# Kernel tuning notes

Measured on AMD Instinct MI355X. Metric: run time of the kernel, lower is better.

The kernel has to match this reference:

```python
import jax, jax.numpy as jnp
import numpy as np

D_MODEL = 1024
NUM_HEADS = 16
HEAD_DIM = D_MODEL // NUM_HEADS
LN_EPS = 1e-5


def setup_inputs() -> dict:
    key = jax.random.key(0)
    ks = jax.random.split(key, 10)
    B, S, D = 4, 2048, D_MODEL
    scale = 1.0 / np.sqrt(D)
    inp = {
        'x': jax.random.normal(ks[0], (B, S, D), dtype=jnp.float32),
        'attention_mask': jnp.ones((B, S), dtype=jnp.float32),
        'Wq': jax.random.normal(ks[1], (D, D), dtype=jnp.float32) * scale,
        'bq': jnp.zeros((D,), dtype=jnp.float32),
        'Wk': jax.random.normal(ks[2], (D, D), dtype=jnp.float32) * scale,
        'bk': jnp.zeros((D,), dtype=jnp.float32),
        'Wv': jax.random.normal(ks[3], (D, D), dtype=jnp.float32) * scale,
        'bv': jnp.zeros((D,), dtype=jnp.float32),
        'Wo': jax.random.normal(ks[4], (D, D), dtype=jnp.float32) * scale,
        'bo': jnp.zeros((D,), dtype=jnp.float32),
        'ln_gamma': jnp.ones((D,), dtype=jnp.float32),
        'ln_beta': jnp.zeros((D,), dtype=jnp.float32),
    }
    return inp


def reference(x, attention_mask, Wq, bq, Wk, bk, Wv, bv, Wo, bo, ln_gamma, ln_beta):
    B, S, D = x.shape
    H, Hd = NUM_HEADS, HEAD_DIM
    identity = x
    # LayerNorm (eps matches torch default 1e-5)
    mu = jnp.mean(x, axis=-1, keepdims=True)
    var = jnp.mean(jnp.square(x - mu), axis=-1, keepdims=True)
    xn = (x - mu) / jnp.sqrt(var + LN_EPS) * ln_gamma + ln_beta
    # projections (torch Linear: x @ W.T + b); weights here stored as [out,in]-compatible square
    q = (xn @ Wq.T + bq).reshape(B, S, H, Hd).transpose(0, 2, 1, 3)  # [B,H,S,Hd]
    k = (xn @ Wk.T + bk).reshape(B, S, H, Hd).transpose(0, 2, 1, 3)
    v = (xn @ Wv.T + bv).reshape(B, S, H, Hd).transpose(0, 2, 1, 3)
    scores = jnp.einsum('bhqd,bhkd->bhqk', q, k) / jnp.sqrt(jnp.float32(Hd))
    # padding mask: [B,S] -> additive [B,1,1,S]
    add_mask = (1.0 - attention_mask)[:, None, None, :] * -10000.0
    scores = scores + add_mask
    # causal mask (strict upper triangle -> -inf)
    causal = jnp.triu(jnp.ones((S, S), dtype=bool), k=1)
    scores = jnp.where(causal[None, None, :, :], -jnp.inf, scores)
    attn = jax.nn.softmax(scores, axis=-1)
    out = jnp.einsum('bhqk,bhkd->bhqd', attn, v)  # [B,H,S,Hd]
    out = out.transpose(0, 2, 1, 3).reshape(B, S, D)
    out = out @ Wo.T + bo
    return identity + out
```

## Files before the change

### kernel.cpp

```cpp
#include <hip/hip_runtime.h>

#define D 1024
#define NH 16
#define HD 64
#define SEQ 2048
#define BATCH 4
#define LN_EPS 1e-5f
#define LOG2E 1.44269504088896f

typedef __attribute__((ext_vector_type(8))) __bf16 bf16x8;
typedef __attribute__((ext_vector_type(4))) float f32x4;

__device__ __forceinline__ ushort f2bf(float f) {
    union { float f; uint u; } c; c.f = f;
    uint u = c.u + 0x7fffu + ((c.u >> 16) & 1u);
    return (ushort)(u >> 16);
}

__device__ __forceinline__ void gl_lds16(const ushort* g, ushort* lds) {
    __builtin_amdgcn_global_load_lds(
        (const __attribute__((address_space(1))) void*)g,
        (__attribute__((address_space(3))) void*)lds, 16, 0, 0);
}

__global__ __launch_bounds__(256) void cvt4(const float* __restrict__ w0,
    const float* __restrict__ w1, const float* __restrict__ w2,
    const float* __restrict__ w3, ushort* __restrict__ out, int n)
{
    int sel = blockIdx.y;
    const float* in = sel == 0 ? w0 : (sel == 1 ? w1 : (sel == 2 ? w2 : w3));
    int i = (blockIdx.x * 256 + threadIdx.x) * 4;
    if (i < n) {
        float4 v = *(const float4*)(in + i);
        ushort4 o;
        o.x = f2bf(v.x); o.y = f2bf(v.y); o.z = f2bf(v.z); o.w = f2bf(v.w);
        *(ushort4*)(out + (size_t)sel * n + i) = o;
    }
}

__global__ __launch_bounds__(256) void ln_kernel(const float* __restrict__ x,
    const float* __restrict__ gamma, const float* __restrict__ beta,
    ushort* __restrict__ xn)
{
    int row = blockIdx.x;
    int tid = threadIdx.x;
    float4 v = ((const float4*)(x + (size_t)row * D))[tid];
    float s = v.x + v.y + v.z + v.w;
#pragma unroll
    for (int off = 32; off > 0; off >>= 1) s += __shfl_down(s, off, 64);
    __shared__ float red1[4], red2[4];
    int wid = tid >> 6, lane = tid & 63;
    if (lane == 0) red1[wid] = s;
    __syncthreads();
    float mean = (red1[0] + red1[1] + red1[2] + red1[3]) * (1.0f / D);
    float dx = v.x - mean, dy = v.y - mean, dz = v.z - mean, dw = v.w - mean;
    float ss = dx * dx + dy * dy + dz * dz + dw * dw;
#pragma unroll
    for (int off = 32; off > 0; off >>= 1) ss += __shfl_down(ss, off, 64);
    if (lane == 0) red2[wid] = ss;
    __syncthreads();
    float var = (red2[0] + red2[1] + red2[2] + red2[3]) * (1.0f / D);
    float rstd = rsqrtf(var + LN_EPS);
    float4 g = ((const float4*)gamma)[tid];
    float4 b = ((const float4*)beta)[tid];
    ushort4 o;
    o.x = f2bf(dx * rstd * g.x + b.x);
    o.y = f2bf(dy * rstd * g.y + b.y);
    o.z = f2bf(dz * rstd * g.z + b.z);
    o.w = f2bf(dw * rstd * g.w + b.w);
    ((ushort4*)(xn + (size_t)row * D))[tid] = o;
}

#define BM 128
#define BKK 64

__global__ __launch_bounds__(256) void gemm_qkv(
    const ushort* __restrict__ A,
    const ushort* __restrict__ W,
    const float* __restrict__ bq, const float* __restrict__ bk,
    const float* __restrict__ bv,
    ushort* __restrict__ Cq, ushort* __restrict__ Ck,
    ushort* __restrict__ CvT,
    int M, int K)
{
    __shared__ ushort As[BM * BKK];
    __shared__ ushort Ws[BM * BKK];
    const int tid = threadIdx.x;
    const int lane = tid & 63;
    const int wave = tid >> 6;
    const int wr = wave >> 1, wc = wave & 1;
    const int m0 = blockIdx.y * BM;
    const int n0g = blockIdx.x * BM;
    const int region = n0g >> 10;
    const int n0l = n0g & 1023;
    const float* bias = region == 0 ? bq : (region == 1 ? bk : bv);
    const int fr = lane & 15, quad = lane >> 4;
    const int r8 = lane >> 3, c8 = lane & 7;
    const int gc8 = c8 ^ r8;
    const int swf = fr & 7;

    const ushort* gA = A + (size_t)(m0 + wave * 32 + r8) * K + gc8 * 8;
    const ushort* gW = W + (size_t)(n0g + wave * 32 + r8) * K + gc8 * 8;
    ushort* ldsA = As + (wave * 32) * BKK;
    ushort* ldsW = Ws + (wave * 32) * BKK;

    f32x4 acc[4][4] = {};

    for (int k0 = 0; k0 < K; k0 += BKK) {
        __syncthreads();
#pragma unroll
        for (int t = 0; t < 4; ++t) {
            gl_lds16(gA + (size_t)t * 8 * K + k0, ldsA + t * 8 * BKK);
            gl_lds16(gW + (size_t)t * 8 * K + k0, ldsW + t * 8 * BKK);
        }
        __syncthreads();
#pragma unroll
        for (int kh = 0; kh < 2; ++kh) {
            bf16x8 af[4], bf[4];
            const int co = ((kh * 4 + quad) ^ swf) * 8;
#pragma unroll
            for (int i = 0; i < 4; ++i) {
                af[i] = *(const bf16x8*)&As[(wr * 64 + i * 16 + fr) * BKK + co];
                bf[i] = *(const bf16x8*)&Ws[(wc * 64 + i * 16 + fr) * BKK + co];
            }
#pragma unroll
            for (int i = 0; i < 4; ++i)
#pragma unroll
                for (int j = 0; j < 4; ++j)
                    acc[i][j] = __builtin_amdgcn_mfma_f32_16x16x32_bf16(af[i], bf[j], acc[i][j], 0, 0, 0);
        }
    }

#pragma unroll
    for (int j = 0; j < 4; ++j) {
        int col = n0l + wc * 64 + j * 16 + fr;
        float bvl = bias[col];
#pragma unroll
        for (int i = 0; i < 4; ++i) {
#pragma unroll
            for (int r = 0; r < 4; ++r) {
                int row = m0 + wr * 64 + i * 16 + quad * 4 + r;
                ushort hv = f2bf(acc[i][j][r] + bvl);
                if (region == 0) {
                    Cq[(size_t)row * 1024 + col] = hv;
                } else if (region == 1) {
                    Ck[(size_t)row * 1024 + col] = hv;
                } else {
                    int bb = row >> 11, s = row & 2047;
                    int hh = col >> 6, d = col & 63;
                    CvT[(((size_t)bb * NH + hh) * HD + d) * SEQ + s] = hv;
                }
            }
        }
    }
}

__global__ __launch_bounds__(256) void gemm_out(
    const ushort* __restrict__ A, const ushort* __restrict__ W,
    const float* __restrict__ bias, const float* __restrict__ resid,
    float* __restrict__ Cf, int M, int N, int K)
{
    __shared__ ushort As[BM * BKK];
    __shared__ ushort Ws[BM * BKK];
    const int tid = threadIdx.x;
    const int lane = tid & 63;
    const int wave = tid >> 6;
    const int wr = wave >> 1, wc = wave & 1;
    const int m0 = blockIdx.y * BM, n0 = blockIdx.x * BM;
    const int fr = lane & 15, quad = lane >> 4;
    const int r8 = lane >> 3, c8 = lane & 7;
    const int gc8 = c8 ^ r8;
    const int swf = fr & 7;

    const ushort* gA = A + (size_t)(m0 + wave * 32 + r8) * K + gc8 * 8;
    const ushort* gW = W + (size_t)(n0 + wave * 32 + r8) * K + gc8 * 8;
    ushort* ldsA = As + (wave * 32) * BKK;
    ushort* ldsW = Ws + (wave * 32) * BKK;

    f32x4 acc[4][4] = {};

    for (int k0 = 0; k0 < K; k0 += BKK) {
        __syncthreads();
#pragma unroll
        for (int t = 0; t < 4; ++t) {
            gl_lds16(gA + (size_t)t * 8 * K + k0, ldsA + t * 8 * BKK);
            gl_lds16(gW + (size_t)t * 8 * K + k0, ldsW + t * 8 * BKK);
        }
        __syncthreads();
#pragma unroll
        for (int kh = 0; kh < 2; ++kh) {
            bf16x8 af[4], bf[4];
            const int co = ((kh * 4 + quad) ^ swf) * 8;
#pragma unroll
            for (int i = 0; i < 4; ++i) {
                af[i] = *(const bf16x8*)&As[(wr * 64 + i * 16 + fr) * BKK + co];
                bf[i] = *(const bf16x8*)&Ws[(wc * 64 + i * 16 + fr) * BKK + co];
            }
#pragma unroll
            for (int i = 0; i < 4; ++i)
#pragma unroll
                for (int j = 0; j < 4; ++j)
                    acc[i][j] = __builtin_amdgcn_mfma_f32_16x16x32_bf16(af[i], bf[j], acc[i][j], 0, 0, 0);
        }
    }

#pragma unroll
    for (int j = 0; j < 4; ++j) {
        int col = n0 + wc * 64 + j * 16 + fr;
        float bvl = bias[col];
#pragma unroll
        for (int i = 0; i < 4; ++i) {
#pragma unroll
            for (int r = 0; r < 4; ++r) {
                int row = m0 + wr * 64 + i * 16 + quad * 4 + r;
                Cf[(size_t)row * N + col] =
                    acc[i][j][r] + bvl + resid[(size_t)row * N + col];
            }
        }
    }
}

#define PSP 72
__global__ __launch_bounds__(256, 3) void flash_mfma(
    const ushort* __restrict__ Q, const ushort* __restrict__ K,
    const ushort* __restrict__ VtG, const float* __restrict__ mask,
    ushort* __restrict__ O)
{
    const int bx = blockIdx.x, h = blockIdx.y, b = blockIdx.z;
    __shared__ ushort Ks[64 * 64];
    __shared__ ushort Vt[64 * 64];
    __shared__ ushort Ps[128 * PSP];
    const int tid = threadIdx.x;
    const int lane = tid & 63, wave = tid >> 6;
    const int fr = lane & 15, quad = lane >> 4;
    const int srow = tid >> 3;
    const int sc8 = tid & 7;
    const int g8 = sc8 ^ (srow & 7);
    const int swf = fr & 7;

    const ushort* gK0 = K + (size_t)(b * SEQ) * D + h * HD + (size_t)srow * D + g8 * 8;
    const ushort* gK1 = gK0 + (size_t)32 * D;
    const ushort* gV0 = VtG + ((size_t)(b * NH + h) * HD + srow) * SEQ + g8 * 8;
    const ushort* gV1 = gV0 + (size_t)32 * SEQ;
    const float* mrow = mask + (size_t)b * SEQ;
    const float SCALE2 = 0.125f * LOG2E;
    const float MASKC = -10000.0f * LOG2E;

    for (int phase = 0; phase < 2; ++phase) {
        const int qt = phase ? (15 - bx) : bx;
        const int q0 = qt * 128;
        bf16x8 qf[2][2];
#pragma unroll
        for (int s = 0; s < 2; ++s) {
            const ushort* qptr = Q + ((size_t)(b * SEQ + q0 + s * 64 + wave * 16 + fr)) * D
                                   + h * HD + quad * 8;
            qf[s][0] = *(const bf16x8*)(qptr);
            qf[s][1] = *(const bf16x8*)(qptr + 32);
        }

        f32x4 oacc[2][4] = {};
        float lsum[2][4] = {};
        const int nkb = 2 * qt + 2;

        for (int kb = 0; kb < nkb; ++kb) {
            __syncthreads();
            gl_lds16(gK0 + (size_t)kb * 64 * D, Ks + wave * 512);
            gl_lds16(gK1 + (size_t)kb * 64 * D, Ks + 2048 + wave * 512);
            gl_lds16(gV0 + kb * 64, Vt + wave * 512);
            gl_lds16(gV1 + kb * 64, Vt + 2048 + wave * 512);
            f32x4 mv[4];
#pragma unroll
            for (int jt = 0; jt < 4; ++jt)
                mv[jt] = ((const f32x4*)(mrow + kb * 64))[jt * 4 + quad];
            __syncthreads();

            const bool s0act = (kb <= 2 * qt);

            f32x4 sacc[2][4] = {};
#pragma unroll
            for (int jt = 0; jt < 4; ++jt) {
                const int rb = (jt * 16 + fr) * 64;
                bf16x8 kf0 = *(const bf16x8*)&Ks[rb + ((quad) ^ swf) * 8];
                bf16x8 kf1 = *(const bf16x8*)&Ks[rb + ((4 + quad) ^ swf) * 8];
                sacc[0][jt] = __builtin_amdgcn_mfma_f32_16x16x32_bf16(kf0, qf[0][0], sacc[0][jt], 0, 0, 0);
                sacc[0][jt] = __builtin_amdgcn_mfma_f32_16x16x32_bf16(kf1, qf[0][1], sacc[0][jt], 0, 0, 0);
                sacc[1][jt] = __builtin_amdgcn_mfma_f32_16x16x32_bf16(kf0, qf[1][0], sacc[1][jt], 0, 0, 0);
                sacc[1][jt] = __builtin_amdgcn_mfma_f32_16x16x32_bf16(kf1, qf[1][1], sacc[1][jt], 0, 0, 0);
            }

            float padd[4][4];
#pragma unroll
            for (int jt = 0; jt < 4; ++jt)
#pragma unroll
                for (int r = 0; r < 4; ++r)
                    padd[jt][r] = fmaf(mv[jt][r], -MASKC, MASKC);
            const int ql = wave * 16 + fr;
#pragma unroll
            for (int s = 0; s < 2; ++s) {
                if (s == 0 && !s0act) continue;
                const bool diag = (kb == 2 * qt + s);
#pragma unroll
                for (int jt = 0; jt < 4; ++jt) {
                    float p[4];
#pragma unroll
                    for (int r = 0; r < 4; ++r) {
                        float v = fmaf(sacc[s][jt][r], SCALE2, padd[jt][r]);
                        if (diag) {
                            int keyl = jt * 16 + quad * 4 + r;
                            v = (keyl > ql) ? -1e30f : v;
                        }
                        float e = exp2f(v);
                        e = __uint_as_float(__float_as_uint(e) & 0xffff0000u);
                        p[r] = e;
                        lsum[s][r] += e;
                    }
                    uint lo = (__float_as_uint(p[0]) >> 16) | (__float_as_uint(p[1]) & 0xffff0000u);
                    uint hi = (__float_as_uint(p[2]) >> 16) | (__float_as_uint(p[3]) & 0xffff0000u);
                    union { uint2 u; ushort4 us; } pu;
                    pu.u.x = lo; pu.u.y = hi;
                    *(ushort4*)&Ps[(s * 64 + wave * 16 + fr) * PSP + jt * 16 + quad * 4] = pu.us;
                }
            }

            bf16x8 pa[2][2];
#pragma unroll
            for (int s = 0; s < 2; ++s) {
                pa[s][0] = *(const bf16x8*)&Ps[(s * 64 + wave * 16 + fr) * PSP + quad * 8];
                pa[s][1] = *(const bf16x8*)&Ps[(s * 64 + wave * 16 + fr) * PSP + 32 + quad * 8];
            }
#pragma unroll
            for (int dt = 0; dt < 4; ++dt) {
                const int rb = (dt * 16 + fr) * 64;
                bf16x8 vf0 = *(const bf16x8*)&Vt[rb + ((quad) ^ swf) * 8];
                bf16x8 vf1 = *(const bf16x8*)&Vt[rb + ((4 + quad) ^ swf) * 8];
                if (s0act) {
                    oacc[0][dt] = __builtin_amdgcn_mfma_f32_16x16x32_bf16(pa[0][0], vf0, oacc[0][dt], 0, 0, 0);
                    oacc[0][dt] = __builtin_amdgcn_mfma_f32_16x16x32_bf16(pa[0][1], vf1, oacc[0][dt], 0, 0, 0);
                }
                oacc[1][dt] = __builtin_amdgcn_mfma_f32_16x16x32_bf16(pa[1][0], vf0, oacc[1][dt], 0, 0, 0);
                oacc[1][dt] = __builtin_amdgcn_mfma_f32_16x16x32_bf16(pa[1][1], vf1, oacc[1][dt], 0, 0, 0);
            }
        }

#pragma unroll
        for (int s = 0; s < 2; ++s) {
            float lt = (lsum[s][0] + lsum[s][1]) + (lsum[s][2] + lsum[s][3]);
            lt += __shfl_xor(lt, 16, 64);
            lt += __shfl_xor(lt, 32, 64);
            float linv[4];
#pragma unroll
            for (int r = 0; r < 4; ++r)
                linv[r] = 1.0f / __shfl(lt, quad * 4 + r, 64);
#pragma unroll
            for (int dt = 0; dt < 4; ++dt)
#pragma unroll
                for (int r = 0; r < 4; ++r) {
                    int q = q0 + s * 64 + wave * 16 + quad * 4 + r;
                    O[((size_t)(b * SEQ + q)) * D + h * HD + dt * 16 + fr] =
                        f2bf(oacc[s][dt][r] * linv[r]);
                }
        }
    }
}

extern "C" void kernel_launch(void* const* d_in, const int* in_sizes, int n_in,
                              void* d_out, int out_size, void* d_ws, size_t ws_size,
                              hipStream_t stream)
{
    const float* x     = (const float*)d_in[0];
    const float* amask = (const float*)d_in[1];
    const float* Wq    = (const float*)d_in[2];
    const float* bq    = (const float*)d_in[3];
    const float* Wk    = (const float*)d_in[4];
    const float* bk    = (const float*)d_in[5];
    const float* Wv    = (const float*)d_in[6];
    const float* bv    = (const float*)d_in[7];
    const float* Wo    = (const float*)d_in[8];
    const float* bo    = (const float*)d_in[9];
    const float* gamma = (const float*)d_in[10];
    const float* beta  = (const float*)d_in[11];
    float* out = (float*)d_out;

    const size_t MROWS = (size_t)BATCH * SEQ;
    const size_t MB = 1024 * 1024;
    char* ws = (char*)d_ws;
    ushort* Qb    = (ushort*)(ws);
    ushort* Kb    = (ushort*)(ws + 16 * MB);
    ushort* Vtb   = (ushort*)(ws + 32 * MB);
    ushort* xn_bf = (ushort*)(ws + 48 * MB);
    ushort* Wq_bf = (ushort*)(ws + 64 * MB);
    ushort* Wo_bf = (ushort*)(ws + 70 * MB);
    ushort* attn_bf = xn_bf;

    const int WN = D * D;
    cvt4<<<dim3(WN / 1024, 4), 256, 0, stream>>>(Wq, Wk, Wv, Wo, Wq_bf, WN);

    ln_kernel<<<dim3((unsigned)MROWS), 256, 0, stream>>>(x, gamma, beta, xn_bf);

    gemm_qkv<<<dim3(24, 64), 256, 0, stream>>>(xn_bf, Wq_bf, bq, bk, bv,
                                               Qb, Kb, Vtb, (int)MROWS, D);

    flash_mfma<<<dim3(8, NH, BATCH), 256, 0, stream>>>(Qb, Kb, Vtb, amask, attn_bf);

    gemm_out<<<dim3(8, 64), 256, 0, stream>>>(attn_bf, Wo_bf, bo, x, out,
                                              (int)MROWS, D, D);
}
```

Measured before the change: 315.5 us.

## Double-buffer LDS tiles in QKV, output GEMMs and flash attention

Gives the two GEMM kernels and the flash attention kernel ping-pong LDS buffers. The next K-tile (or K/V block) is issued as an async global-to-LDS load before the MFMA work on the current tile, and each iteration needs one barrier instead of two. The aim is to hide global memory latency behind matrix math. In exchange, the GEMM kernels use twice the shared memory, which can lower how many blocks fit on each CU.

```diff
diff --git a/kernel.cpp b/kernel.cpp
--- a/kernel.cpp
+++ b/kernel.cpp
@@ -83,8 +83,8 @@
     ushort* __restrict__ CvT,
     int M, int K)
 {
-    __shared__ ushort As[BM * BKK];
-    __shared__ ushort Ws[BM * BKK];
+    __shared__ ushort As[2][BM * BKK];
+    __shared__ ushort Ws[2][BM * BKK];
     const int tid = threadIdx.x;
     const int lane = tid & 63;
     const int wave = tid >> 6;
@@ -101,27 +101,35 @@
 
     const ushort* gA = A + (size_t)(m0 + wave * 32 + r8) * K + gc8 * 8;
     const ushort* gW = W + (size_t)(n0g + wave * 32 + r8) * K + gc8 * 8;
-    ushort* ldsA = As + (wave * 32) * BKK;
-    ushort* ldsW = Ws + (wave * 32) * BKK;
+    const int ldso = (wave * 32) * BKK;
 
     f32x4 acc[4][4] = {};
 
+#pragma unroll
+    for (int t = 0; t < 4; ++t) {
+        gl_lds16(gA + (size_t)t * 8 * K, &As[0][ldso + t * 8 * BKK]);
+        gl_lds16(gW + (size_t)t * 8 * K, &Ws[0][ldso + t * 8 * BKK]);
+    }
+    __syncthreads();
+
     for (int k0 = 0; k0 < K; k0 += BKK) {
-        __syncthreads();
-#pragma unroll
-        for (int t = 0; t < 4; ++t) {
-            gl_lds16(gA + (size_t)t * 8 * K + k0, ldsA + t * 8 * BKK);
-            gl_lds16(gW + (size_t)t * 8 * K + k0, ldsW + t * 8 * BKK);
-        }
-        __syncthreads();
+        const int cur = (k0 >> 6) & 1;
+        if (k0 + BKK < K) {
+            const int nxt = cur ^ 1;
+#pragma unroll
+            for (int t = 0; t < 4; ++t) {
+                gl_lds16(gA + (size_t)t * 8 * K + k0 + BKK, &As[nxt][ldso + t * 8 * BKK]);
+                gl_lds16(gW + (size_t)t * 8 * K + k0 + BKK, &Ws[nxt][ldso + t * 8 * BKK]);
+            }
+        }
 #pragma unroll
         for (int kh = 0; kh < 2; ++kh) {
             bf16x8 af[4], bf[4];
             const int co = ((kh * 4 + quad) ^ swf) * 8;
 #pragma unroll
             for (int i = 0; i < 4; ++i) {
-                af[i] = *(const bf16x8*)&As[(wr * 64 + i * 16 + fr) * BKK + co];
-                bf[i] = *(const bf16x8*)&Ws[(wc * 64 + i * 16 + fr) * BKK + co];
+                af[i] = *(const bf16x8*)&As[cur][(wr * 64 + i * 16 + fr) * BKK + co];
+                bf[i] = *(const bf16x8*)&Ws[cur][(wc * 64 + i * 16 + fr) * BKK + co];
             }
 #pragma unroll
             for (int i = 0; i < 4; ++i)
@@ -129,6 +137,7 @@
                 for (int j = 0; j < 4; ++j)
                     acc[i][j] = __builtin_amdgcn_mfma_f32_16x16x32_bf16(af[i], bf[j], acc[i][j], 0, 0, 0);
         }
+        __syncthreads();
     }
 
 #pragma unroll
@@ -160,8 +169,8 @@
     const float* __restrict__ bias, const float* __restrict__ resid,
     float* __restrict__ Cf, int M, int N, int K)
 {
-    __shared__ ushort As[BM * BKK];
-    __shared__ ushort Ws[BM * BKK];
+    __shared__ ushort As[2][BM * BKK];
+    __shared__ ushort Ws[2][BM * BKK];
     const int tid = threadIdx.x;
     const int lane = tid & 63;
     const int wave = tid >> 6;
@@ -174,27 +183,35 @@
 
     const ushort* gA = A + (size_t)(m0 + wave * 32 + r8) * K + gc8 * 8;
     const ushort* gW = W + (size_t)(n0 + wave * 32 + r8) * K + gc8 * 8;
-    ushort* ldsA = As + (wave * 32) * BKK;
-    ushort* ldsW = Ws + (wave * 32) * BKK;
+    const int ldso = (wave * 32) * BKK;
 
     f32x4 acc[4][4] = {};
 
+#pragma unroll
+    for (int t = 0; t < 4; ++t) {
+        gl_lds16(gA + (size_t)t * 8 * K, &As[0][ldso + t * 8 * BKK]);
+        gl_lds16(gW + (size_t)t * 8 * K, &Ws[0][ldso + t * 8 * BKK]);
+    }
+    __syncthreads();
+
     for (int k0 = 0; k0 < K; k0 += BKK) {
-        __syncthreads();
-#pragma unroll
-        for (int t = 0; t < 4; ++t) {
-            gl_lds16(gA + (size_t)t * 8 * K + k0, ldsA + t * 8 * BKK);
-            gl_lds16(gW + (size_t)t * 8 * K + k0, ldsW + t * 8 * BKK);
-        }
-        __syncthreads();
+        const int cur = (k0 >> 6) & 1;
+        if (k0 + BKK < K) {
+            const int nxt = cur ^ 1;
+#pragma unroll
+            for (int t = 0; t < 4; ++t) {
+                gl_lds16(gA + (size_t)t * 8 * K + k0 + BKK, &As[nxt][ldso + t * 8 * BKK]);
+                gl_lds16(gW + (size_t)t * 8 * K + k0 + BKK, &Ws[nxt][ldso + t * 8 * BKK]);
+            }
+        }
 #pragma unroll
         for (int kh = 0; kh < 2; ++kh) {
             bf16x8 af[4], bf[4];
             const int co = ((kh * 4 + quad) ^ swf) * 8;
 #pragma unroll
             for (int i = 0; i < 4; ++i) {
-                af[i] = *(const bf16x8*)&As[(wr * 64 + i * 16 + fr) * BKK + co];
-                bf[i] = *(const bf16x8*)&Ws[(wc * 64 + i * 16 + fr) * BKK + co];
+                af[i] = *(const bf16x8*)&As[cur][(wr * 64 + i * 16 + fr) * BKK + co];
+                bf[i] = *(const bf16x8*)&Ws[cur][(wc * 64 + i * 16 + fr) * BKK + co];
             }
 #pragma unroll
             for (int i = 0; i < 4; ++i)
@@ -202,6 +219,7 @@
                 for (int j = 0; j < 4; ++j)
                     acc[i][j] = __builtin_amdgcn_mfma_f32_16x16x32_bf16(af[i], bf[j], acc[i][j], 0, 0, 0);
         }
+        __syncthreads();
     }
 
 #pragma unroll
@@ -227,8 +245,8 @@
     ushort* __restrict__ O)
 {
     const int bx = blockIdx.x, h = blockIdx.y, b = blockIdx.z;
-    __shared__ ushort Ks[64 * 64];
-    __shared__ ushort Vt[64 * 64];
+    __shared__ ushort Ks[2][64 * 64];
+    __shared__ ushort Vt[2][64 * 64];
     __shared__ ushort Ps[128 * PSP];
     const int tid = threadIdx.x;
     const int lane = tid & 63, wave = tid >> 6;
@@ -262,17 +280,25 @@
         float lsum[2][4] = {};
         const int nkb = 2 * qt + 2;
 
+        gl_lds16(gK0, &Ks[0][wave * 512]);
+        gl_lds16(gK1, &Ks[0][2048 + wave * 512]);
+        gl_lds16(gV0, &Vt[0][wave * 512]);
+        gl_lds16(gV1, &Vt[0][2048 + wave * 512]);
+        __syncthreads();
+
         for (int kb = 0; kb < nkb; ++kb) {
-            __syncthreads();
-            gl_lds16(gK0 + (size_t)kb * 64 * D, Ks + wave * 512);
-            gl_lds16(gK1 + (size_t)kb * 64 * D, Ks + 2048 + wave * 512);
-            gl_lds16(gV0 + kb * 64, Vt + wave * 512);
-            gl_lds16(gV1 + kb * 64, Vt + 2048 + wave * 512);
+            const int cur = kb & 1;
+            if (kb + 1 < nkb) {
+                const int nxt = cur ^ 1;
+                gl_lds16(gK0 + (size_t)(kb + 1) * 64 * D, &Ks[nxt][wave * 512]);
+                gl_lds16(gK1 + (size_t)(kb + 1) * 64 * D, &Ks[nxt][2048 + wave * 512]);
+                gl_lds16(gV0 + (kb + 1) * 64, &Vt[nxt][wave * 512]);
+                gl_lds16(gV1 + (kb + 1) * 64, &Vt[nxt][2048 + wave * 512]);
+            }
             f32x4 mv[4];
 #pragma unroll
             for (int jt = 0; jt < 4; ++jt)
                 mv[jt] = ((const f32x4*)(mrow + kb * 64))[jt * 4 + quad];
-            __syncthreads();
 
             const bool s0act = (kb <= 2 * qt);
 
@@ -280,8 +306,8 @@
 #pragma unroll
             for (int jt = 0; jt < 4; ++jt) {
                 const int rb = (jt * 16 + fr) * 64;
-                bf16x8 kf0 = *(const bf16x8*)&Ks[rb + ((quad) ^ swf) * 8];
-                bf16x8 kf1 = *(const bf16x8*)&Ks[rb + ((4 + quad) ^ swf) * 8];
+                bf16x8 kf0 = *(const bf16x8*)&Ks[cur][rb + ((quad) ^ swf) * 8];
+                bf16x8 kf1 = *(const bf16x8*)&Ks[cur][rb + ((4 + quad) ^ swf) * 8];
                 sacc[0][jt] = __builtin_amdgcn_mfma_f32_16x16x32_bf16(kf0, qf[0][0], sacc[0][jt], 0, 0, 0);
                 sacc[0][jt] = __builtin_amdgcn_mfma_f32_16x16x32_bf16(kf1, qf[0][1], sacc[0][jt], 0, 0, 0);
                 sacc[1][jt] = __builtin_amdgcn_mfma_f32_16x16x32_bf16(kf0, qf[1][0], sacc[1][jt], 0, 0, 0);
@@ -331,8 +357,8 @@
 #pragma unroll
             for (int dt = 0; dt < 4; ++dt) {
                 const int rb = (dt * 16 + fr) * 64;
-                bf16x8 vf0 = *(const bf16x8*)&Vt[rb + ((quad) ^ swf) * 8];
-                bf16x8 vf1 = *(const bf16x8*)&Vt[rb + ((4 + quad) ^ swf) * 8];
+                bf16x8 vf0 = *(const bf16x8*)&Vt[cur][rb + ((quad) ^ swf) * 8];
+                bf16x8 vf1 = *(const bf16x8*)&Vt[cur][rb + ((4 + quad) ^ swf) * 8];
                 if (s0act) {
                     oacc[0][dt] = __builtin_amdgcn_mfma_f32_16x16x32_bf16(pa[0][0], vf0, oacc[0][dt], 0, 0, 0);
                     oacc[0][dt] = __builtin_amdgcn_mfma_f32_16x16x32_bf16(pa[0][1], vf1, oacc[0][dt], 0, 0, 0);
@@ -340,6 +366,7 @@
                 oacc[1][dt] = __builtin_amdgcn_mfma_f32_16x16x32_bf16(pa[1][0], vf0, oacc[1][dt], 0, 0, 0);
                 oacc[1][dt] = __builtin_amdgcn_mfma_f32_16x16x32_bf16(pa[1][1], vf1, oacc[1][dt], 0, 0, 0);
             }
+            __syncthreads();
         }
 
 #pragma unroll
```

Result: no change. 312.9 us (-0.8%).
